# Performance work log

Measured on AMD Instinct MI355X. Metric: run time of the kernel, lower is better.

The kernel has to match this reference:

```python
import jax, jax.numpy as jnp
import numpy as np

EPS = 1e-5

def _bn(x, g, b, m, v):
    # eval-mode batchnorm over channel axis 1 of NCHW
    scale = g * jax.lax.rsqrt(v + EPS)
    return x * scale[None, :, None, None] + (b - m * scale)[None, :, None, None]

def _dwconv3x3(x, w):
    # x: [N,C,H,W], w: [C,1,3,3] depthwise, stride 1, pad 1
    C = x.shape[1]
    return jax.lax.conv_general_dilated(
        x, w, window_strides=(1, 1), padding=((1, 1), (1, 1)),
        dimension_numbers=('NCHW', 'OIHW', 'NCHW'), feature_group_count=C)

def setup_inputs() -> dict:
    key = jax.random.key(0)
    ks = jax.random.split(key, 16)
    N, C, H, W = 32, 96, 56, 56
    Hd = 576  # hidden_dim = round(96 * 6)
    inp = {}
    inp['x'] = jax.random.normal(ks[0], (N, C, H, W), jnp.float32)
    inp['w1'] = jax.random.normal(ks[1], (Hd, C), jnp.float32) * 0.05
    inp['g1'] = jax.random.uniform(ks[2], (Hd,), jnp.float32, 0.5, 1.5)
    inp['b1'] = jax.random.normal(ks[3], (Hd,), jnp.float32) * 0.1
    inp['m1'] = jax.random.normal(ks[4], (Hd,), jnp.float32) * 0.1
    inp['v1'] = jax.random.uniform(ks[5], (Hd,), jnp.float32, 0.5, 1.5)
    inp['wdw'] = jax.random.normal(ks[6], (Hd, 1, 3, 3), jnp.float32) * 0.1
    inp['gdw'] = jax.random.uniform(ks[7], (Hd,), jnp.float32, 0.5, 1.5)
    inp['bdw'] = jax.random.normal(ks[8], (Hd,), jnp.float32) * 0.1
    inp['mdw'] = jax.random.normal(ks[9], (Hd,), jnp.float32) * 0.1
    inp['vdw'] = jax.random.uniform(ks[10], (Hd,), jnp.float32, 0.5, 1.5)
    inp['w2'] = jax.random.normal(ks[11], (C, Hd), jnp.float32) * 0.05
    inp['g2'] = jax.random.uniform(ks[12], (C,), jnp.float32, 0.5, 1.5)
    inp['b2'] = jax.random.normal(ks[13], (C,), jnp.float32) * 0.1
    inp['m2'] = jax.random.normal(ks[14], (C,), jnp.float32) * 0.1
    inp['v2'] = jax.random.uniform(ks[15], (C,), jnp.float32, 0.5, 1.5)
    return inp

def reference(x, w1, g1, b1, m1, v1, wdw, gdw, bdw, mdw, vdw, w2, g2, b2, m2, v2):
    # expand 1x1 conv (as GEMM) + BN + ReLU
    h = jnp.einsum('oc,bchw->bohw', w1, x)
    h = jax.nn.relu(_bn(h, g1, b1, m1, v1))
    # depthwise 3x3 + BN + ReLU
    h = _dwconv3x3(h, wdw)
    h = jax.nn.relu(_bn(h, gdw, bdw, mdw, vdw))
    # project 1x1 conv + BN (no ReLU)
    out = jnp.einsum('oc,bchw->bohw', w2, h)
    out = _bn(out, g2, b2, m2, v2)
    # residual (stride==1, inp==oup)
    return x + out
```

## Files before the change

kernel.cpp:

```cpp
#include <hip/hip_runtime.h>
#include <hip/hip_bf16.h>

typedef __attribute__((ext_vector_type(8))) short bf16x8;
typedef __attribute__((ext_vector_type(4))) float f32x4;
typedef unsigned short u16;
typedef unsigned int u32;

#define EPS 1e-5f
#define CIN 96
#define HD 576
#define HW 3136
#define NB 32

#define XTS   96
#define HC_OFF 0
#define HCS   338
#define H2_OFF (64 * HCS * 2)
#define H2S   72
#define BN_OFF (H2_OFF + 224 * H2S * 2)
#define SMEM_BYTES (BN_OFF + 2496 * 4)

__device__ __forceinline__ u16 f2bf(float f) {
  u32 u = __builtin_bit_cast(u32, f);
  u32 r = u + 0x7fffu + ((u >> 16) & 1u);
  return (u16)(r >> 16);
}
__device__ __forceinline__ float bf2f(u16 h) {
  return __builtin_bit_cast(float, (u32)h << 16);
}

__global__ __launch_bounds__(256) void prep_kernel(
    const float* __restrict__ w1, const float* __restrict__ w2,
    const float* __restrict__ g1, const float* __restrict__ b1,
    const float* __restrict__ m1, const float* __restrict__ v1,
    const float* __restrict__ gdw, const float* __restrict__ bdw,
    const float* __restrict__ mdw, const float* __restrict__ vdw,
    const float* __restrict__ g2, const float* __restrict__ b2,
    const float* __restrict__ m2, const float* __restrict__ v2,
    u16* __restrict__ w1b, u16* __restrict__ w2b, float* __restrict__ bn)
{
  int i = blockIdx.x * 256 + threadIdx.x;
  if (i < HD * CIN) {
    w1b[i] = f2bf(w1[i]);
    w2b[i] = f2bf(w2[i]);
  }
  if (i < HD) {
    float s = g1[i] * rsqrtf(v1[i] + EPS);
    bn[i] = s;
    bn[HD + i] = b1[i] - m1[i] * s;
    float sd = gdw[i] * rsqrtf(vdw[i] + EPS);
    bn[2 * HD + i] = sd;
    bn[3 * HD + i] = bdw[i] - mdw[i] * sd;
  }
  if (i < CIN) {
    float s2 = g2[i] * rsqrtf(v2[i] + EPS);
    bn[4 * HD + i] = s2;
    bn[4 * HD + CIN + i] = b2[i] - m2[i] * s2;
  }
}

__global__ __launch_bounds__(448, 2) void fused_kernel(
    const float* __restrict__ x, const u16* __restrict__ w1b,
    const u16* __restrict__ w2b, const float* __restrict__ wdw,
    const float* __restrict__ bnp, float* __restrict__ out)
{
  extern __shared__ __align__(16) char smem[];
  u16*   Xt  = (u16*)(smem);
  u16*   Hc  = (u16*)(smem + HC_OFF);
  u16*   H2c = (u16*)(smem + H2_OFF);
  float* bnS = (float*)(smem + BN_OFF);

  const int tid = threadIdx.x;
  const int r0  = blockIdx.x * 4;
  const int b   = blockIdx.y;
  const int l   = tid & 63;
  const int w   = tid >> 6;
  const int lr  = l & 15;
  const int kq  = l >> 4;
  const int kb  = kq * 8;

  for (int i = tid; i < 2496; i += 448) bnS[i] = bnp[i];

  const float* xb = x + (size_t)b * CIN * HW;
  const int pbase = (r0 - 1) * 56;
#pragma unroll
  for (int it = 0; it < 9; ++it) {
    int i = it * 448 + tid;
    int px = i % 336;
    int g  = i / 336;
    int gpx = pbase + px;
    gpx = gpx < 0 ? 0 : (gpx > HW - 1 ? HW - 1 : gpx);
    const float* xp = xb + (size_t)(g * 8) * HW + gpx;
    bf16x8 pk;
#pragma unroll
    for (int j = 0; j < 8; ++j) pk[j] = (short)f2bf(xp[(size_t)j * HW]);
    *(bf16x8*)&Xt[px * XTS + g * 8] = pk;
  }
  __syncthreads();

  bf16x8 xf[3][3];
#pragma unroll
  for (int t = 0; t < 3; ++t)
#pragma unroll
    for (int ks = 0; ks < 3; ++ks)
      xf[t][ks] = *(const bf16x8*)&Xt[((w * 3 + t) * 16 + lr) * XTS + ks * 32 + kb];
  __syncthreads();

  f32x4 pacc[2][6] = {};

  for (int kc = 0; kc < 9; ++kc) {
    const int ch0 = kc * 64;
    bf16x8 af[4][3];
#pragma unroll
    for (int mt = 0; mt < 4; ++mt)
#pragma unroll
      for (int ks = 0; ks < 3; ++ks)
        af[mt][ks] = *(const bf16x8*)&w1b[(size_t)(ch0 + mt * 16 + lr) * CIN + ks * 32 + kb];

    f32x4 bsc[4], bsh[4];
#pragma unroll
    for (int mt = 0; mt < 4; ++mt) {
      bsc[mt] = *(const f32x4*)&bnS[ch0 + mt * 16 + kq * 4];
      bsh[mt] = *(const f32x4*)&bnS[HD + ch0 + mt * 16 + kq * 4];
    }

#pragma unroll
    for (int t = 0; t < 3; ++t) {
      f32x4 ea[4] = {};
#pragma unroll
      for (int ks = 0; ks < 3; ++ks) {
        ea[0] = __builtin_amdgcn_mfma_f32_16x16x32_bf16(af[0][ks], xf[t][ks], ea[0], 0, 0, 0);
        ea[1] = __builtin_amdgcn_mfma_f32_16x16x32_bf16(af[1][ks], xf[t][ks], ea[1], 0, 0, 0);
        ea[2] = __builtin_amdgcn_mfma_f32_16x16x32_bf16(af[2][ks], xf[t][ks], ea[2], 0, 0, 0);
        ea[3] = __builtin_amdgcn_mfma_f32_16x16x32_bf16(af[3][ks], xf[t][ks], ea[3], 0, 0, 0);
      }
      const int hpx = (w * 3 + t) * 16 + lr;
#pragma unroll
      for (int mt = 0; mt < 4; ++mt)
#pragma unroll
        for (int i = 0; i < 4; ++i) {
          int chl = mt * 16 + kq * 4 + i;
          float v = fmaxf(ea[mt][i] * bsc[mt][i] + bsh[mt][i], 0.f);
          Hc[chl * HCS + hpx] = f2bf(v);
        }
    }
    __syncthreads();

#pragma unroll
    for (int it = 0; it < 2; ++it) {
      int t   = it * 448 + tid;
      int chl = t & 63;
      int cg  = t >> 6;
      int c0  = cg * 4;
      int gch = ch0 + chl;
      float wk[9];
#pragma unroll
      for (int k = 0; k < 9; ++k) wk[k] = wdw[gch * 9 + k];
      const float sdw = bnS[2 * HD + gch], hdw = bnS[3 * HD + gch];

      float win[6][8];
#pragma unroll
      for (int hr = 0; hr < 6; ++hr) {
        int grow = r0 - 1 + hr;
        bool rv = (grow >= 0) && (grow < 56);
        const u16* rp = &Hc[chl * HCS + hr * 56];
#pragma unroll
        for (int k2 = 0; k2 < 4; ++k2) {
          int cb = c0 - 2 + k2 * 2;
          u32 pr = (rv && cb >= 0) ? *(const u32*)(rp + cb) : 0u;
          win[hr][k2 * 2]     = bf2f((u16)pr);
          win[hr][k2 * 2 + 1] = bf2f((u16)(pr >> 16));
        }
        if (c0 + 4 >= 56) win[hr][6] = 0.f;
      }
#pragma unroll
      for (int orr = 0; orr < 4; ++orr) {
        float a4[4] = {0.f, 0.f, 0.f, 0.f};
#pragma unroll
        for (int dy = 0; dy < 3; ++dy)
#pragma unroll
          for (int j = 0; j < 4; ++j)
#pragma unroll
            for (int dx = 0; dx < 3; ++dx)
              a4[j] += wk[dy * 3 + dx] * win[orr + dy][j + dx + 1];
#pragma unroll
        for (int j = 0; j < 4; ++j) {
          float v = fmaxf(a4[j] * sdw + hdw, 0.f);
          H2c[(orr * 56 + c0 + j) * H2S + chl] = f2bf(v);
        }
      }
    }
    __syncthreads();

    bf16x8 pa[6][2];
#pragma unroll
    for (int mt = 0; mt < 6; ++mt)
#pragma unroll
      for (int ks = 0; ks < 2; ++ks)
        pa[mt][ks] = *(const bf16x8*)&w2b[(size_t)(mt * 16 + lr) * HD + ch0 + ks * 32 + kb];
#pragma unroll
    for (int ntl = 0; ntl < 2; ++ntl) {
      int pt = w * 2 + ntl;
      bf16x8 pb[2];
#pragma unroll
      for (int ks = 0; ks < 2; ++ks)
        pb[ks] = *(const bf16x8*)&H2c[(pt * 16 + lr) * H2S + ks * 32 + kb];
#pragma unroll
      for (int ks = 0; ks < 2; ++ks)
#pragma unroll
        for (int mt = 0; mt < 6; ++mt)
          pacc[ntl][mt] = __builtin_amdgcn_mfma_f32_16x16x32_bf16(pa[mt][ks], pb[ks], pacc[ntl][mt], 0, 0, 0);
    }
  }

  const float* xr = x   + (size_t)b * CIN * HW + r0 * 56;
  float*       ob = out + (size_t)b * CIN * HW + r0 * 56;
#pragma unroll
  for (int ntl = 0; ntl < 2; ++ntl) {
    int opx = (w * 2 + ntl) * 16 + lr;
#pragma unroll
    for (int mt = 0; mt < 6; ++mt)
#pragma unroll
      for (int i = 0; i < 4; ++i) {
        int c = mt * 16 + kq * 4 + i;
        float v = pacc[ntl][mt][i] * bnS[4 * HD + c] + bnS[4 * HD + CIN + c];
        size_t idx = (size_t)c * HW + opx;
        ob[idx] = v + xr[idx];
      }
  }
}

extern "C" void kernel_launch(void* const* d_in, const int* in_sizes, int n_in,
                              void* d_out, int out_size, void* d_ws, size_t ws_size,
                              hipStream_t stream) {
  const float* x   = (const float*)d_in[0];
  const float* w1  = (const float*)d_in[1];
  const float* g1  = (const float*)d_in[2];
  const float* b1  = (const float*)d_in[3];
  const float* m1  = (const float*)d_in[4];
  const float* v1  = (const float*)d_in[5];
  const float* wdw = (const float*)d_in[6];
  const float* gdw = (const float*)d_in[7];
  const float* bdw = (const float*)d_in[8];
  const float* mdw = (const float*)d_in[9];
  const float* vdw = (const float*)d_in[10];
  const float* w2  = (const float*)d_in[11];
  const float* g2  = (const float*)d_in[12];
  const float* b2  = (const float*)d_in[13];
  const float* m2  = (const float*)d_in[14];
  const float* v2  = (const float*)d_in[15];
  float* out = (float*)d_out;

  char* ws = (char*)d_ws;
  u16*   w1b = (u16*)ws;
  u16*   w2b = (u16*)(ws + 2 * (size_t)HD * CIN);
  float* bnp = (float*)(ws + 4 * (size_t)HD * CIN);

  (void)hipFuncSetAttribute((const void*)fused_kernel,
                            hipFuncAttributeMaxDynamicSharedMemorySize, SMEM_BYTES);

  prep_kernel<<<dim3((HD * CIN + 255) / 256), 256, 0, stream>>>(
      w1, w2, g1, b1, m1, v1, gdw, bdw, mdw, vdw, g2, b2, m2, v2, w1b, w2b, bnp);

  fused_kernel<<<dim3(14, NB), 448, SMEM_BYTES, stream>>>(x, w1b, w2b, wdw, bnp, out);
}
```

Before: 249.9 us.

## Drop LDS BN-param copy, pad Xt stride, hoist dw weights, raise occupancy bound

Removes the shared-memory copy of the BN parameters and reads them directly from global memory, shrinking LDS use. Pads the Xt row stride from 96 to 104 elements to reduce LDS bank conflicts. Hoists the depthwise weight and BN loads out of the inner two-iteration loop, which is valid because each thread's channel is the same in both iterations. Raises the launch-bounds min-blocks hint from 2 to 4 to target higher occupancy. The tighter register budget risks spilling, and at roughly 75 KB of LDS per block only about two blocks can fit on a CU anyway.

```diff
diff --git a/kernel.cpp b/kernel.cpp
--- a/kernel.cpp
+++ b/kernel.cpp
@@ -12,13 +12,12 @@
 #define HW 3136
 #define NB 32
 
-#define XTS   96
+#define XTS   104
 #define HC_OFF 0
 #define HCS   338
 #define H2_OFF (64 * HCS * 2)
 #define H2S   72
-#define BN_OFF (H2_OFF + 224 * H2S * 2)
-#define SMEM_BYTES (BN_OFF + 2496 * 4)
+#define SMEM_BYTES (H2_OFF + 224 * H2S * 2)
 
 __device__ __forceinline__ u16 f2bf(float f) {
   u32 u = __builtin_bit_cast(u32, f);
@@ -59,16 +58,15 @@
   }
 }
 
-__global__ __launch_bounds__(448, 2) void fused_kernel(
+__global__ __launch_bounds__(448, 4) void fused_kernel(
     const float* __restrict__ x, const u16* __restrict__ w1b,
     const u16* __restrict__ w2b, const float* __restrict__ wdw,
     const float* __restrict__ bnp, float* __restrict__ out)
 {
   extern __shared__ __align__(16) char smem[];
-  u16*   Xt  = (u16*)(smem);
-  u16*   Hc  = (u16*)(smem + HC_OFF);
-  u16*   H2c = (u16*)(smem + H2_OFF);
-  float* bnS = (float*)(smem + BN_OFF);
+  u16* Xt  = (u16*)(smem);
+  u16* Hc  = (u16*)(smem + HC_OFF);
+  u16* H2c = (u16*)(smem + H2_OFF);
 
   const int tid = threadIdx.x;
   const int r0  = blockIdx.x * 4;
@@ -79,8 +77,6 @@
   const int kq  = l >> 4;
   const int kb  = kq * 8;
 
-  for (int i = tid; i < 2496; i += 448) bnS[i] = bnp[i];
-
   const float* xb = x + (size_t)b * CIN * HW;
   const int pbase = (r0 - 1) * 56;
 #pragma unroll
@@ -106,10 +102,18 @@
       xf[t][ks] = *(const bf16x8*)&Xt[((w * 3 + t) * 16 + lr) * XTS + ks * 32 + kb];
   __syncthreads();
 
+  const int chl_dw = tid & 63;
   f32x4 pacc[2][6] = {};
 
   for (int kc = 0; kc < 9; ++kc) {
     const int ch0 = kc * 64;
+
+    const int gch_dw = ch0 + chl_dw;
+    float wk[9];
+#pragma unroll
+    for (int k = 0; k < 9; ++k) wk[k] = wdw[gch_dw * 9 + k];
+    const float sdw = bnp[2 * HD + gch_dw], hdw = bnp[3 * HD + gch_dw];
+
     bf16x8 af[4][3];
 #pragma unroll
     for (int mt = 0; mt < 4; ++mt)
@@ -120,8 +124,8 @@
     f32x4 bsc[4], bsh[4];
 #pragma unroll
     for (int mt = 0; mt < 4; ++mt) {
-      bsc[mt] = *(const f32x4*)&bnS[ch0 + mt * 16 + kq * 4];
-      bsh[mt] = *(const f32x4*)&bnS[HD + ch0 + mt * 16 + kq * 4];
+      bsc[mt] = *(const f32x4*)&bnp[ch0 + mt * 16 + kq * 4];
+      bsh[mt] = *(const f32x4*)&bnp[HD + ch0 + mt * 16 + kq * 4];
     }
 
 #pragma unroll
@@ -148,22 +152,15 @@
 
 #pragma unroll
     for (int it = 0; it < 2; ++it) {
-      int t   = it * 448 + tid;
-      int chl = t & 63;
-      int cg  = t >> 6;
-      int c0  = cg * 4;
-      int gch = ch0 + chl;
-      float wk[9];
-#pragma unroll
-      for (int k = 0; k < 9; ++k) wk[k] = wdw[gch * 9 + k];
-      const float sdw = bnS[2 * HD + gch], hdw = bnS[3 * HD + gch];
+      int cg = (tid >> 6) + it * 7;
+      int c0 = cg * 4;
 
       float win[6][8];
 #pragma unroll
       for (int hr = 0; hr < 6; ++hr) {
         int grow = r0 - 1 + hr;
         bool rv = (grow >= 0) && (grow < 56);
-        const u16* rp = &Hc[chl * HCS + hr * 56];
+        const u16* rp = &Hc[chl_dw * HCS + hr * 56];
 #pragma unroll
         for (int k2 = 0; k2 < 4; ++k2) {
           int cb = c0 - 2 + k2 * 2;
@@ -186,7 +183,7 @@
 #pragma unroll
         for (int j = 0; j < 4; ++j) {
           float v = fmaxf(a4[j] * sdw + hdw, 0.f);
-          H2c[(orr * 56 + c0 + j) * H2S + chl] = f2bf(v);
+          H2c[(orr * 56 + c0 + j) * H2S + chl_dw] = f2bf(v);
         }
       }
     }
@@ -216,17 +213,20 @@
   const float* xr = x   + (size_t)b * CIN * HW + r0 * 56;
   float*       ob = out + (size_t)b * CIN * HW + r0 * 56;
 #pragma unroll
-  for (int ntl = 0; ntl < 2; ++ntl) {
-    int opx = (w * 2 + ntl) * 16 + lr;
-#pragma unroll
-    for (int mt = 0; mt < 6; ++mt)
+  for (int mt = 0; mt < 6; ++mt) {
+    f32x4 s2 = *(const f32x4*)&bnp[4 * HD + mt * 16 + kq * 4];
+    f32x4 h2 = *(const f32x4*)&bnp[4 * HD + CIN + mt * 16 + kq * 4];
+#pragma unroll
+    for (int ntl = 0; ntl < 2; ++ntl) {
+      int opx = (w * 2 + ntl) * 16 + lr;
 #pragma unroll
       for (int i = 0; i < 4; ++i) {
         int c = mt * 16 + kq * 4 + i;
-        float v = pacc[ntl][mt][i] * bnS[4 * HD + c] + bnS[4 * HD + CIN + c];
+        float v = pacc[ntl][mt][i] * s2[i] + h2[i];
         size_t idx = (size_t)c * HW + opx;
         ob[idx] = v + xr[idx];
       }
+    }
   }
 }
 
```

Result: slower. 334.7 us (+33.9%).
